# Optimization experiments

Hardware: AMD Instinct MI355X
Metric: run time of the kernel (lower is better)

Reference implementation:

```python
import jax, jax.numpy as jnp
import numpy as np

B, S, H, D = 2, 2048, 16, 64
HID = H * D


def setup_inputs() -> dict:
    key = jax.random.key(0)
    ks = jax.random.split(key, 9)
    s = 1.0 / np.sqrt(HID)
    return {
        "x": jax.random.normal(ks[0], (B, S, HID), dtype=jnp.float32),
        "Wq": jax.random.normal(ks[1], (HID, HID), dtype=jnp.float32) * s,
        "bq": jax.random.normal(ks[2], (HID,), dtype=jnp.float32) * s,
        "Wk": jax.random.normal(ks[3], (HID, HID), dtype=jnp.float32) * s,
        "bk": jax.random.normal(ks[4], (HID,), dtype=jnp.float32) * s,
        "Wv": jax.random.normal(ks[5], (HID, HID), dtype=jnp.float32) * s,
        "bv": jax.random.normal(ks[6], (HID,), dtype=jnp.float32) * s,
        "Wp": jax.random.normal(ks[7], (HID, HID), dtype=jnp.float32) * s,
        "bp": jax.random.normal(ks[8], (HID,), dtype=jnp.float32) * s,
    }


def reference(x, Wq, bq, Wk, bk, Wv, bv, Wp, bp):
    b, s, hid = x.shape
    d = hid // H
    # linear projections (torch Linear: x @ W.T + b), split heads -> [b, h, s, d]
    def heads(y):
        return y.reshape(b, s, H, d).transpose(0, 2, 1, 3)
    q = heads(x @ Wq.T + bq)
    k = heads(x @ Wk.T + bk)
    v = heads(x @ Wv.T + bv)
    scale = 1.0 / np.sqrt(d).astype(np.float32)
    att = jnp.einsum("bhqd,bhkd->bhqk", q, k) * scale
    causal = jnp.tril(jnp.ones((s, s), dtype=bool))  # [s, s]
    att = jnp.where(causal[None, None], att, -jnp.inf)
    att = jax.nn.softmax(att, axis=-1)
    y = jnp.einsum("bhqk,bhkd->bhqd", att, v)
    y = y.transpose(0, 2, 1, 3).reshape(b, s, hid)
    return y @ Wp.T + bp
```

## Files before the change

kernel.cpp:

```cpp
#include <hip/hip_runtime.h>


typedef unsigned short u16;
typedef float f32x4 __attribute__((ext_vector_type(4)));
typedef __bf16 bf16x8 __attribute__((ext_vector_type(8)));
typedef unsigned short u16x4 __attribute__((ext_vector_type(4)));
typedef unsigned short u16x8 __attribute__((ext_vector_type(8)));

constexpr int Bn = 2, SEQ = 2048, NH = 16, HD = 64, HID = 1024;
constexpr size_t NX = (size_t)Bn * SEQ * HID;
constexpr size_t NW = (size_t)HID * HID;

__device__ __forceinline__ u16 f2bf(float f) {
  unsigned u = __float_as_uint(f);
  u += 0x7fff + ((u >> 16) & 1);
  return (u16)(u >> 16);
}

__device__ __forceinline__ f32x4 mfma16(bf16x8 a, bf16x8 b, f32x4 c) {
  return __builtin_amdgcn_mfma_f32_16x16x32_bf16(a, b, c, 0, 0, 0);
}

__device__ __forceinline__ void gload16(const u16* g, u16* l) {
  __builtin_amdgcn_global_load_lds(
      (const __attribute__((address_space(1))) unsigned int*)(const void*)g,
      (__attribute__((address_space(3))) unsigned int*)(void*)l, 16, 0, 0);
}

__global__ void cvt_all(const float* __restrict__ x,
                        const float* __restrict__ Wq, const float* __restrict__ Wk,
                        const float* __restrict__ Wv, const float* __restrict__ Wp,
                        u16* __restrict__ xb, u16* __restrict__ wqb, u16* __restrict__ wkb,
                        u16* __restrict__ wvb, u16* __restrict__ wpb) {
  size_t i = ((size_t)blockIdx.x * blockDim.x + threadIdx.x) * 4;
  const float* s; u16* d; size_t off;
  if (i < NX) { s = x; d = xb; off = i; }
  else {
    size_t k = i - NX;
    int id = (int)(k >> 20);
    off = k & (NW - 1);
    s = (id == 0) ? Wq : (id == 1) ? Wk : (id == 2) ? Wv : Wp;
    d = (id == 0) ? wqb : (id == 1) ? wkb : (id == 2) ? wvb : wpb;
  }
  float4 v = *reinterpret_cast<const float4*>(s + off);
  u16x4 o = {f2bf(v.x), f2bf(v.y), f2bf(v.z), f2bf(v.w)};
  *reinterpret_cast<u16x4*>(d + off) = o;
}

__global__ __launch_bounds__(256) void qkv_gemm(
    const u16* __restrict__ A,
    const u16* __restrict__ W0, const u16* __restrict__ W1, const u16* __restrict__ W2,
    const float* __restrict__ b0, const float* __restrict__ b1, const float* __restrict__ b2,
    u16* __restrict__ out0, u16* __restrict__ out1, u16* __restrict__ out2)
{
  constexpr int K = HID;
  __shared__ u16 As[128 * 32];
  __shared__ u16 Bs[128 * 32];
  const int tid = threadIdx.x;
  const int lane = tid & 63, w = tid >> 6;
  const int wr = w >> 1, wc = w & 1;
  const int l15 = lane & 15, g = lane >> 4;
  const int m0 = blockIdx.x * 128;
  const int n0g = blockIdx.y * 128;
  const int id = n0g >> 10;
  const int n0 = n0g & (HID - 1);
  const u16* Bm = (id == 0) ? W0 : (id == 1) ? W1 : W2;
  const float* bias = (id == 0) ? b0 : (id == 1) ? b1 : b2;
  u16* out = (id == 0) ? out0 : (id == 1) ? out1 : out2;

  f32x4 acc[4][4] = {};

  for (int kt = 0; kt < K; kt += 32) {
    __syncthreads();
#pragma unroll
    for (int i = 0; i < 2; i++) {
      int chunk = tid + 256 * i;
      int r = chunk >> 2, c = (chunk & 3) << 3;
      gload16(&A[(size_t)(m0 + r) * K + kt + c], &As[(size_t)chunk * 8]);
      gload16(&Bm[(size_t)(n0 + r) * K + kt + c], &Bs[(size_t)chunk * 8]);
    }
    __syncthreads();
    bf16x8 af[4], bfr[4];
#pragma unroll
    for (int mi = 0; mi < 4; mi++)
      af[mi] = *reinterpret_cast<const bf16x8*>(&As[(wr * 64 + mi * 16 + l15) * 32 + g * 8]);
#pragma unroll
    for (int ni = 0; ni < 4; ni++)
      bfr[ni] = *reinterpret_cast<const bf16x8*>(&Bs[(wc * 64 + ni * 16 + l15) * 32 + g * 8]);
#pragma unroll
    for (int mi = 0; mi < 4; mi++)
#pragma unroll
      for (int ni = 0; ni < 4; ni++)
        acc[mi][ni] = mfma16(af[mi], bfr[ni], acc[mi][ni]);
  }

  float bv[4];
#pragma unroll
  for (int ni = 0; ni < 4; ni++) bv[ni] = bias[n0 + wc * 64 + ni * 16 + l15];

#pragma unroll
  for (int mi = 0; mi < 4; mi++)
#pragma unroll
    for (int ni = 0; ni < 4; ni++)
#pragma unroll
      for (int r = 0; r < 4; r++) {
        int gm = m0 + wr * 64 + mi * 16 + g * 4 + r;
        int gn = n0 + wc * 64 + ni * 16 + l15;
        int bb = gm >> 11, sq = gm & (SEQ - 1);
        int hh = gn >> 6, d = gn & 63;
        size_t off = (id == 2)
            ? (((size_t)(bb * NH + hh) * HD + d) * SEQ + sq)
            : (((size_t)(bb * NH + hh) * SEQ + sq) * HD + d);
        out[off] = f2bf(acc[mi][ni][r] + bv[ni]);
      }
}

__global__ __launch_bounds__(256) void gemm_out(
    const u16* __restrict__ A, const u16* __restrict__ Bm,
    const float* __restrict__ bias, float* __restrict__ out)
{
  constexpr int K = HID, N = HID;
  __shared__ u16 As[64 * 32];
  __shared__ u16 Bs[128 * 32];
  const int tid = threadIdx.x;
  const int lane = tid & 63, w = tid >> 6;
  const int l15 = lane & 15, g = lane >> 4;
  const int m0 = blockIdx.x * 64, n0 = blockIdx.y * 128;

  f32x4 acc[4][2] = {};

  for (int kt = 0; kt < K; kt += 32) {
    __syncthreads();
    {
      int r = tid >> 2, c = (tid & 3) << 3;
      gload16(&A[(size_t)(m0 + r) * K + kt + c], &As[(size_t)tid * 8]);
    }
#pragma unroll
    for (int i = 0; i < 2; i++) {
      int chunk = tid + 256 * i;
      int r = chunk >> 2, c = (chunk & 3) << 3;
      gload16(&Bm[(size_t)(n0 + r) * K + kt + c], &Bs[(size_t)chunk * 8]);
    }
    __syncthreads();
    bf16x8 af[4], bfr[2];
#pragma unroll
    for (int mi = 0; mi < 4; mi++)
      af[mi] = *reinterpret_cast<const bf16x8*>(&As[(mi * 16 + l15) * 32 + g * 8]);
#pragma unroll
    for (int ni = 0; ni < 2; ni++)
      bfr[ni] = *reinterpret_cast<const bf16x8*>(&Bs[(w * 32 + ni * 16 + l15) * 32 + g * 8]);
#pragma unroll
    for (int mi = 0; mi < 4; mi++)
#pragma unroll
      for (int ni = 0; ni < 2; ni++)
        acc[mi][ni] = mfma16(af[mi], bfr[ni], acc[mi][ni]);
  }

  float bv[2];
#pragma unroll
  for (int ni = 0; ni < 2; ni++) bv[ni] = bias[n0 + w * 32 + ni * 16 + l15];

#pragma unroll
  for (int mi = 0; mi < 4; mi++)
#pragma unroll
    for (int ni = 0; ni < 2; ni++)
#pragma unroll
      for (int r = 0; r < 4; r++) {
        int gm = m0 + mi * 16 + g * 4 + r;
        int gn = n0 + w * 32 + ni * 16 + l15;
        out[(size_t)gm * N + gn] = acc[mi][ni][r] + bv[ni];
      }
}

__global__ __launch_bounds__(256, 4) void attn_kernel(
    const u16* __restrict__ Q, const u16* __restrict__ Kt,
    const u16* __restrict__ Vt, u16* __restrict__ Y)
{
  __shared__ u16 smK[2][4096];
  __shared__ u16 smV[2][4096];
  const int tid = threadIdx.x;
  const int lane = tid & 63, w = tid >> 6;
  const int l15 = lane & 15, g = lane >> 4;
  const int h = blockIdx.y, b = blockIdx.z;
  const int jb = blockIdx.x;
  const int xs = l15 & 7;

  const size_t bh = (size_t)(b * NH + h);
  const u16* Qp = Q + bh * SEQ * HD;
  const u16* Kp = Kt + bh * SEQ * HD;
  const u16* Vp = Vt + bh * HD * SEQ;

  int srow[2], sslot[2];
#pragma unroll
  for (int it = 0; it < 2; it++) {
    int idx = it * 256 + tid;
    srow[it] = idx >> 3;
    sslot[it] = (idx & 7) ^ (srow[it] & 7);
  }
  auto stage = [&](int buf, int kt) {
#pragma unroll
    for (int it = 0; it < 2; it++) {
      int idx = it * 256 + tid;
      gload16(Kp + (size_t)(kt + srow[it]) * HD + sslot[it] * 8, &smK[buf][idx * 8]);
      gload16(Vp + (size_t)srow[it] * SEQ + kt + sslot[it] * 8, &smV[buf][idx * 8]);
    }
  };

  const float QSC = 0.125f * 1.44269504088896f;
  const float NEG = -__builtin_inff();

  for (int pi = 0; pi < 2; pi++) {
    const int tile = pi ? (31 - jb) : jb;
    const int nt = tile + 1;
    const int q0 = tile * 64 + w * 16;
    const int qg = q0 + l15;

    __syncthreads();
    stage(0, 0);

    bf16x8 qf[2];
#pragma unroll
    for (int hf = 0; hf < 2; hf++) {
      bf16x8 tq = *reinterpret_cast<const bf16x8*>(Qp + (size_t)qg * HD + hf * 32 + g * 8);
#pragma unroll
      for (int jj = 0; jj < 8; jj++) qf[hf][jj] = (__bf16)((float)tq[jj] * QSC);
    }

    float m_run = NEG, l_run = 0.0f;
    f32x4 o[4] = {};

    for (int t = 0; t < nt; t++) {
      const int kt = t * 64;
      const int buf = t & 1;
      __syncthreads();
      if (t + 1 < nt) stage(buf ^ 1, kt + 64);

      f32x4 sa[4];
#pragma unroll
      for (int sub = 0; sub < 4; sub++) {
        int row = sub * 16 + l15;
        bf16x8 k0 = *reinterpret_cast<const bf16x8*>(&smK[buf][row * 64 + ((0 + g) ^ xs) * 8]);
        bf16x8 k1 = *reinterpret_cast<const bf16x8*>(&smK[buf][row * 64 + ((4 + g) ^ xs) * 8]);
        f32x4 a = {0.f, 0.f, 0.f, 0.f};
        a = mfma16(k0, qf[0], a);
        a = mfma16(k1, qf[1], a);
        sa[sub] = a;
      }

      float p[16];
      if (t == nt - 1) {
#pragma unroll
        for (int sub = 0; sub < 4; sub++)
#pragma unroll
          for (int r = 0; r < 4; r++) {
            int key = kt + sub * 16 + g * 4 + r;
            p[sub * 4 + r] = (key <= qg) ? sa[sub][r] : NEG;
          }
      } else {
#pragma unroll
        for (int sub = 0; sub < 4; sub++)
#pragma unroll
          for (int r = 0; r < 4; r++) p[sub * 4 + r] = sa[sub][r];
      }

      float t8[8], t4[4];
#pragma unroll
      for (int i = 0; i < 8; i++) t8[i] = fmaxf(p[i], p[i + 8]);
#pragma unroll
      for (int i = 0; i < 4; i++) t4[i] = fmaxf(t8[i], t8[i + 4]);
      float tmax = fmaxf(fmaxf(t4[0], t4[2]), fmaxf(t4[1], t4[3]));
      tmax = fmaxf(tmax, __shfl_xor(tmax, 16));
      tmax = fmaxf(tmax, __shfl_xor(tmax, 32));

      if (__any(tmax > m_run + 11.0f)) {
        float mnew = fmaxf(m_run, tmax);
        float fs = __builtin_amdgcn_exp2f(m_run - mnew);
        l_run *= fs;
#pragma unroll
        for (int db = 0; db < 4; db++) o[db] *= fs;
        m_run = mnew;
      }

      float pe[16];
      float s4[4] = {0.f, 0.f, 0.f, 0.f};
#pragma unroll
      for (int i = 0; i < 16; i++) {
        pe[i] = __builtin_amdgcn_exp2f(p[i] - m_run);
        s4[i & 3] += pe[i];
      }
      float psum = (s4[0] + s4[1]) + (s4[2] + s4[3]);
      psum += __shfl_xor(psum, 16);
      psum += __shfl_xor(psum, 32);
      l_run += psum;

#pragma unroll
      for (int half = 0; half < 2; half++) {
        bf16x8 pb;
#pragma unroll
        for (int jj = 0; jj < 8; jj++) pb[jj] = (__bf16)pe[8 * half + jj];
        const int s0 = ((4 * half + (g >> 1)) ^ xs) * 8 + 4 * (g & 1);
        const int s1 = ((4 * half + 2 + (g >> 1)) ^ xs) * 8 + 4 * (g & 1);
#pragma unroll
        for (int db = 0; db < 4; db++) {
          int vbase = (db * 16 + l15) * 64;
          u16x4 v0 = *reinterpret_cast<const u16x4*>(&smV[buf][vbase + s0]);
          u16x4 v1 = *reinterpret_cast<const u16x4*>(&smV[buf][vbase + s1]);
          u16x8 vau;
#pragma unroll
          for (int jj = 0; jj < 4; jj++) { vau[jj] = v0[jj]; vau[jj + 4] = v1[jj]; }
          bf16x8 va = __builtin_bit_cast(bf16x8, vau);
          o[db] = mfma16(va, pb, o[db]);
        }
      }
    }

    float rl = 1.0f / l_run;
#pragma unroll
    for (int db = 0; db < 4; db++) {
      u16x4 yo;
#pragma unroll
      for (int r = 0; r < 4; r++) yo[r] = f2bf(o[db][r] * rl);
      *reinterpret_cast<u16x4*>(
          Y + ((size_t)(b * SEQ) + qg) * HID + h * HD + db * 16 + g * 4) = yo;
    }
  }
}

extern "C" void kernel_launch(void* const* d_in, const int* in_sizes, int n_in,
                              void* d_out, int out_size, void* d_ws, size_t ws_size,
                              hipStream_t stream) {
  const float* x  = (const float*)d_in[0];
  const float* Wq = (const float*)d_in[1];
  const float* bq = (const float*)d_in[2];
  const float* Wk = (const float*)d_in[3];
  const float* bk = (const float*)d_in[4];
  const float* Wv = (const float*)d_in[5];
  const float* bv = (const float*)d_in[6];
  const float* Wp = (const float*)d_in[7];
  const float* bp = (const float*)d_in[8];

  u16* ws = (u16*)d_ws;
  u16* xb  = ws; ws += NX;
  u16* wqb = ws; ws += NW;
  u16* wkb = ws; ws += NW;
  u16* wvb = ws; ws += NW;
  u16* wpb = ws; ws += NW;
  u16* Qb  = ws; ws += NX;
  u16* Kb  = ws; ws += NX;
  u16* Vtb = ws; ws += NX;
  u16* Yb  = ws; ws += NX;

  const unsigned cvtBlocks = (unsigned)((NX + 4 * NW) / 4 / 256);
  cvt_all<<<cvtBlocks, 256, 0, stream>>>(x, Wq, Wk, Wv, Wp, xb, wqb, wkb, wvb, wpb);

  qkv_gemm<<<dim3(32, 24), 256, 0, stream>>>(xb, wqb, wkb, wvb, bq, bk, bv, Qb, Kb, Vtb);

  attn_kernel<<<dim3(16, NH, Bn), 256, 0, stream>>>(Qb, Kb, Vtb, Yb);

  gemm_out<<<dim3(64, 8), 256, 0, stream>>>(Yb, wpb, bp, (float*)d_out);
}
```

Baseline: 121.8 us.

## Double-buffer GEMMs, LDS-transpose V store, triple-buffer attention with XCD-aware block mapping

Both GEMM kernels now double-buffer their LDS tiles so the next K-slice loads while the current one is consumed, and grid axes are swapped to change block rasterization. The V projection output is transposed through LDS with an XOR swizzle and written as 16-byte vectors instead of scattered 2-byte stores. The attention kernel moves to a 3-stage K/V ring with explicit vmcnt waits and raw barriers, issues Q loads before staging, and remaps a 1D grid so each XCD handles a few heads for L2 locality. The changes raise LDS use and drop the occupancy hint on attention; the hand-written vmcnt counts must match the number of outstanding loads.

New measurement: 118.9 us. -2.4%, faster.

```diff
diff --git a/kernel.cpp b/kernel.cpp
--- a/kernel.cpp
+++ b/kernel.cpp
@@ -54,32 +54,37 @@
     u16* __restrict__ out0, u16* __restrict__ out1, u16* __restrict__ out2)
 {
   constexpr int K = HID;
-  __shared__ u16 As[128 * 32];
-  __shared__ u16 Bs[128 * 32];
+  __shared__ u16 smem[16384];
   const int tid = threadIdx.x;
   const int lane = tid & 63, w = tid >> 6;
   const int wr = w >> 1, wc = w & 1;
   const int l15 = lane & 15, g = lane >> 4;
-  const int m0 = blockIdx.x * 128;
-  const int n0g = blockIdx.y * 128;
+  const int m0 = blockIdx.y * 128;
+  const int n0g = blockIdx.x * 128;
   const int id = n0g >> 10;
   const int n0 = n0g & (HID - 1);
   const u16* Bm = (id == 0) ? W0 : (id == 1) ? W1 : W2;
   const float* bias = (id == 0) ? b0 : (id == 1) ? b1 : b2;
-  u16* out = (id == 0) ? out0 : (id == 1) ? out1 : out2;
-
-  f32x4 acc[4][4] = {};
-
-  for (int kt = 0; kt < K; kt += 32) {
-    __syncthreads();
+
+  auto stage = [&](int buf, int kt) {
 #pragma unroll
     for (int i = 0; i < 2; i++) {
       int chunk = tid + 256 * i;
       int r = chunk >> 2, c = (chunk & 3) << 3;
-      gload16(&A[(size_t)(m0 + r) * K + kt + c], &As[(size_t)chunk * 8]);
-      gload16(&Bm[(size_t)(n0 + r) * K + kt + c], &Bs[(size_t)chunk * 8]);
-    }
+      gload16(&A[(size_t)(m0 + r) * K + kt + c], &smem[buf * 4096 + chunk * 8]);
+      gload16(&Bm[(size_t)(n0 + r) * K + kt + c], &smem[8192 + buf * 4096 + chunk * 8]);
+    }
+  };
+
+  f32x4 acc[4][4] = {};
+  stage(0, 0);
+
+  for (int ki = 0; ki < 32; ki++) {
+    const int buf = ki & 1;
     __syncthreads();
+    if (ki + 1 < 32) stage(buf ^ 1, (ki + 1) * 32);
+    const u16* As = &smem[buf * 4096];
+    const u16* Bs = &smem[8192 + buf * 4096];
     bf16x8 af[4], bfr[4];
 #pragma unroll
     for (int mi = 0; mi < 4; mi++)
@@ -98,21 +103,50 @@
 #pragma unroll
   for (int ni = 0; ni < 4; ni++) bv[ni] = bias[n0 + wc * 64 + ni * 16 + l15];
 
-#pragma unroll
-  for (int mi = 0; mi < 4; mi++)
-#pragma unroll
-    for (int ni = 0; ni < 4; ni++)
-#pragma unroll
-      for (int r = 0; r < 4; r++) {
-        int gm = m0 + wr * 64 + mi * 16 + g * 4 + r;
-        int gn = n0 + wc * 64 + ni * 16 + l15;
-        int bb = gm >> 11, sq = gm & (SEQ - 1);
-        int hh = gn >> 6, d = gn & 63;
-        size_t off = (id == 2)
-            ? (((size_t)(bb * NH + hh) * HD + d) * SEQ + sq)
-            : (((size_t)(bb * NH + hh) * SEQ + sq) * HD + d);
-        out[off] = f2bf(acc[mi][ni][r] + bv[ni]);
-      }
+  if (id == 2) {
+    __syncthreads();
+#pragma unroll
+    for (int mi = 0; mi < 4; mi++)
+#pragma unroll
+      for (int ni = 0; ni < 4; ni++) {
+        u16x4 pk;
+#pragma unroll
+        for (int r = 0; r < 4; r++) pk[r] = f2bf(acc[mi][ni][r] + bv[ni]);
+        int d_loc = wc * 64 + ni * 16 + l15;
+        int sq_base = wr * 64 + mi * 16 + g * 4;
+        *reinterpret_cast<u16x4*>(
+            &smem[d_loc * 128 + (sq_base ^ ((d_loc & 7) << 4))]) = pk;
+      }
+    __syncthreads();
+    const int bb = m0 >> 11;
+    const int sq0 = m0 & (SEQ - 1);
+#pragma unroll
+    for (int i = 0; i < 8; i++) {
+      int chunk = tid + 256 * i;
+      int d_loc = chunk >> 4;
+      int sqc = (chunk & 15) << 3;
+      u16x8 val = *reinterpret_cast<const u16x8*>(
+          &smem[d_loc * 128 + (sqc ^ ((d_loc & 7) << 4))]);
+      int gn = n0 + d_loc;
+      int hh = gn >> 6, dd = gn & 63;
+      *reinterpret_cast<u16x8*>(
+          &out2[((size_t)(bb * NH + hh) * HD + dd) * SEQ + sq0 + sqc]) = val;
+    }
+  } else {
+    u16* out = (id == 0) ? out0 : out1;
+#pragma unroll
+    for (int mi = 0; mi < 4; mi++)
+#pragma unroll
+      for (int ni = 0; ni < 4; ni++)
+#pragma unroll
+        for (int r = 0; r < 4; r++) {
+          int gm = m0 + wr * 64 + mi * 16 + g * 4 + r;
+          int gn = n0 + wc * 64 + ni * 16 + l15;
+          int bb = gm >> 11, sq = gm & (SEQ - 1);
+          int hh = gn >> 6, d = gn & 63;
+          out[((size_t)(bb * NH + hh) * SEQ + sq) * HD + d] = f2bf(acc[mi][ni][r] + bv[ni]);
+        }
+  }
 }
 
 __global__ __launch_bounds__(256) void gemm_out(
@@ -120,35 +154,40 @@
     const float* __restrict__ bias, float* __restrict__ out)
 {
   constexpr int K = HID, N = HID;
-  __shared__ u16 As[64 * 32];
-  __shared__ u16 Bs[128 * 32];
+  __shared__ u16 As[2][64 * 32];
+  __shared__ u16 Bs[2][128 * 32];
   const int tid = threadIdx.x;
   const int lane = tid & 63, w = tid >> 6;
   const int l15 = lane & 15, g = lane >> 4;
-  const int m0 = blockIdx.x * 64, n0 = blockIdx.y * 128;
-
-  f32x4 acc[4][2] = {};
-
-  for (int kt = 0; kt < K; kt += 32) {
-    __syncthreads();
+  const int m0 = blockIdx.y * 64, n0 = blockIdx.x * 128;
+
+  auto stage = [&](int buf, int kt) {
     {
       int r = tid >> 2, c = (tid & 3) << 3;
-      gload16(&A[(size_t)(m0 + r) * K + kt + c], &As[(size_t)tid * 8]);
+      gload16(&A[(size_t)(m0 + r) * K + kt + c], &As[buf][tid * 8]);
     }
 #pragma unroll
     for (int i = 0; i < 2; i++) {
       int chunk = tid + 256 * i;
       int r = chunk >> 2, c = (chunk & 3) << 3;
-      gload16(&Bm[(size_t)(n0 + r) * K + kt + c], &Bs[(size_t)chunk * 8]);
-    }
+      gload16(&Bm[(size_t)(n0 + r) * K + kt + c], &Bs[buf][chunk * 8]);
+    }
+  };
+
+  f32x4 acc[4][2] = {};
+  stage(0, 0);
+
+  for (int ki = 0; ki < 32; ki++) {
+    const int buf = ki & 1;
     __syncthreads();
+    if (ki + 1 < 32) stage(buf ^ 1, (ki + 1) * 32);
     bf16x8 af[4], bfr[2];
 #pragma unroll
     for (int mi = 0; mi < 4; mi++)
-      af[mi] = *reinterpret_cast<const bf16x8*>(&As[(mi * 16 + l15) * 32 + g * 8]);
+      af[mi] = *reinterpret_cast<const bf16x8*>(&As[buf][(mi * 16 + l15) * 32 + g * 8]);
 #pragma unroll
     for (int ni = 0; ni < 2; ni++)
-      bfr[ni] = *reinterpret_cast<const bf16x8*>(&Bs[(w * 32 + ni * 16 + l15) * 32 + g * 8]);
+      bfr[ni] = *reinterpret_cast<const bf16x8*>(&Bs[buf][(w * 32 + ni * 16 + l15) * 32 + g * 8]);
 #pragma unroll
     for (int mi = 0; mi < 4; mi++)
 #pragma unroll
@@ -172,23 +211,26 @@
       }
 }
 
-__global__ __launch_bounds__(256, 4) void attn_kernel(
+__global__ __launch_bounds__(256) void attn_kernel(
     const u16* __restrict__ Q, const u16* __restrict__ Kt,
     const u16* __restrict__ Vt, u16* __restrict__ Y)
 {
-  __shared__ u16 smK[2][4096];
-  __shared__ u16 smV[2][4096];
+  __shared__ u16 smK[3][4096];
+  __shared__ u16 smV[3][4096];
   const int tid = threadIdx.x;
   const int lane = tid & 63, w = tid >> 6;
   const int l15 = lane & 15, g = lane >> 4;
-  const int h = blockIdx.y, b = blockIdx.z;
-  const int jb = blockIdx.x;
+  const int bid = blockIdx.x;
+  const int xcd = bid & 7, kk = bid >> 3;
+  const int bh = xcd * 4 + (kk >> 4);
+  const int jb = kk & 15;
+  const int b = bh >> 4, h = bh & 15;
   const int xs = l15 & 7;
 
-  const size_t bh = (size_t)(b * NH + h);
-  const u16* Qp = Q + bh * SEQ * HD;
-  const u16* Kp = Kt + bh * SEQ * HD;
-  const u16* Vp = Vt + bh * HD * SEQ;
+  const size_t bhs = (size_t)bh;
+  const u16* Qp = Q + bhs * SEQ * HD;
+  const u16* Kp = Kt + bhs * SEQ * HD;
+  const u16* Vp = Vt + bhs * HD * SEQ;
 
   int srow[2], sslot[2];
 #pragma unroll
@@ -216,14 +258,18 @@
     const int qg = q0 + l15;
 
     __syncthreads();
+
+    bf16x8 tq0 = *reinterpret_cast<const bf16x8*>(Qp + (size_t)qg * HD + g * 8);
+    bf16x8 tq1 = *reinterpret_cast<const bf16x8*>(Qp + (size_t)qg * HD + 32 + g * 8);
+
     stage(0, 0);
+    if (nt > 1) stage(1, 64);
 
     bf16x8 qf[2];
 #pragma unroll
-    for (int hf = 0; hf < 2; hf++) {
-      bf16x8 tq = *reinterpret_cast<const bf16x8*>(Qp + (size_t)qg * HD + hf * 32 + g * 8);
-#pragma unroll
-      for (int jj = 0; jj < 8; jj++) qf[hf][jj] = (__bf16)((float)tq[jj] * QSC);
+    for (int jj = 0; jj < 8; jj++) {
+      qf[0][jj] = (__bf16)((float)tq0[jj] * QSC);
+      qf[1][jj] = (__bf16)((float)tq1[jj] * QSC);
     }
 
     float m_run = NEG, l_run = 0.0f;
@@ -231,16 +277,19 @@
 
     for (int t = 0; t < nt; t++) {
       const int kt = t * 64;
-      const int buf = t & 1;
-      __syncthreads();
-      if (t + 1 < nt) stage(buf ^ 1, kt + 64);
+      const u16* K_ = smK[t % 3];
+      const u16* V_ = smV[t % 3];
+      if (t + 1 < nt) { asm volatile("s_waitcnt vmcnt(4)" ::: "memory"); }
+      else            { asm volatile("s_waitcnt vmcnt(0)" ::: "memory"); }
+      __builtin_amdgcn_s_barrier();
+      if (t + 2 < nt) stage((t + 2) % 3, kt + 128);
 
       f32x4 sa[4];
 #pragma unroll
       for (int sub = 0; sub < 4; sub++) {
         int row = sub * 16 + l15;
-        bf16x8 k0 = *reinterpret_cast<const bf16x8*>(&smK[buf][row * 64 + ((0 + g) ^ xs) * 8]);
-        bf16x8 k1 = *reinterpret_cast<const bf16x8*>(&smK[buf][row * 64 + ((4 + g) ^ xs) * 8]);
+        bf16x8 k0 = *reinterpret_cast<const bf16x8*>(&K_[row * 64 + ((0 + g) ^ xs) * 8]);
+        bf16x8 k1 = *reinterpret_cast<const bf16x8*>(&K_[row * 64 + ((4 + g) ^ xs) * 8]);
         f32x4 a = {0.f, 0.f, 0.f, 0.f};
         a = mfma16(k0, qf[0], a);
         a = mfma16(k1, qf[1], a);
@@ -303,8 +352,8 @@
 #pragma unroll
         for (int db = 0; db < 4; db++) {
           int vbase = (db * 16 + l15) * 64;
-          u16x4 v0 = *reinterpret_cast<const u16x4*>(&smV[buf][vbase + s0]);
-          u16x4 v1 = *reinterpret_cast<const u16x4*>(&smV[buf][vbase + s1]);
+          u16x4 v0 = *reinterpret_cast<const u16x4*>(&V_[vbase + s0]);
+          u16x4 v1 = *reinterpret_cast<const u16x4*>(&V_[vbase + s1]);
           u16x8 vau;
 #pragma unroll
           for (int jj = 0; jj < 4; jj++) { vau[jj] = v0[jj]; vau[jj + 4] = v1[jj]; }
@@ -353,9 +402,9 @@
   const unsigned cvtBlocks = (unsigned)((NX + 4 * NW) / 4 / 256);
   cvt_all<<<cvtBlocks, 256, 0, stream>>>(x, Wq, Wk, Wv, Wp, xb, wqb, wkb, wvb, wpb);
 
-  qkv_gemm<<<dim3(32, 24), 256, 0, stream>>>(xb, wqb, wkb, wvb, bq, bk, bv, Qb, Kb, Vtb);
-
-  attn_kernel<<<dim3(16, NH, Bn), 256, 0, stream>>>(Qb, Kb, Vtb, Yb);
-
-  gemm_out<<<dim3(64, 8), 256, 0, stream>>>(Yb, wpb, bp, (float*)d_out);
-}
+  qkv_gemm<<<dim3(24, 32), 256, 0, stream>>>(xb, wqb, wkb, wvb, bq, bk, bv, Qb, Kb, Vtb);
+
+  attn_kernel<<<dim3(512), 256, 0, stream>>>(Qb, Kb, Vtb, Yb);
+
+  gemm_out<<<dim3(8, 64), 256, 0, stream>>>(Yb, wpb, bp, (float*)d_out);
+}
```
